# Performance work log

Measured on AMD Instinct MI355X. Metric: run time of the kernel, lower is better.

The kernel has to match this reference:

```python
import jax, jax.numpy as jnp
from jax import lax
import numpy as np

K = 5  # length_inter_tile
EPS = 0.01


def _conv(x, w, b):
    y = lax.conv_general_dilated(x, w, (1, 1), ((1, 1), (1, 1)),
                                 dimension_numbers=('NCHW', 'OIHW', 'NCHW'))
    return y + b[None, :, None, None]


def _leaky(x):
    return jnp.where(x >= 0, x, 0.01 * x)


def _unfold(x, k=K):
    # torch F.unfold(x, k, padding=k//2): (b,c,h,w) -> (b, c*k*k, h*w), channel-major ordering
    b, c, h, w = x.shape
    p = k // 2
    xp = jnp.pad(x, ((0, 0), (0, 0), (p, p), (p, p)))
    pat = jnp.stack([xp[:, :, i:i + h, j:j + w] for i in range(k) for j in range(k)], axis=2)
    return pat.reshape(b, c * k * k, h * w)


def _fold(x, c, h, w, k=K):
    # torch F.fold: (b, c*k*k, h*w) -> (b, c, h, w) with overlap-add, padding=k//2
    b = x.shape[0]
    p = k // 2
    xr = x.reshape(b, c, k, k, h, w)
    out = jnp.zeros((b, c, h + 2 * p, w + 2 * p), x.dtype)
    for i in range(k):
        for j in range(k):
            out = out.at[:, :, i:i + h, j:j + w].add(xr[:, :, i, j])
    return out[:, :, p:p + h, p:p + w]


def _mmn(x, axes):
    mn = jnp.min(x, axis=axes, keepdims=True)
    mx = jnp.max(x, axis=axes, keepdims=True)
    return (x - mn) / (mx - mn + 0.001)


def setup_inputs() -> dict:
    key = jax.random.key(0)
    ks = jax.random.split(key, 8)
    b, t, ch_in, h, w = 1, 16, 10, 24, 24
    t_de, ch_de = 16, 12
    sc = 0.02
    return {
        'x': jax.random.normal(ks[0], (b, t, ch_in, h, w), jnp.float32),
        'design': jax.random.uniform(ks[1], (b, t_de, ch_de, h, w), jnp.float32),
        'gt': jax.random.uniform(ks[2], (b, t_de, 3, h, w), jnp.float32),
        'w1': jax.random.normal(ks[3], (1024, 160, 3, 3), jnp.float32) * sc,
        'b1': jnp.zeros((1024,), jnp.float32),
        'w2': jax.random.normal(ks[4], (1024, 1024, 3, 3), jnp.float32) * sc,
        'b2': jnp.zeros((1024,), jnp.float32),
        'w3': jax.random.normal(ks[5], (1024, 1024, 3, 3), jnp.float32) * sc,
        'b3': jnp.zeros((1024,), jnp.float32),
        'wf': jax.random.normal(ks[6], (6400, 1024, 3, 3), jnp.float32) * sc,
        'bf': jnp.zeros((6400,), jnp.float32),
    }


def _forward(x, design, gt, w1, b1, w2, b2, w3, b3, wf, bf):
    b, t, ch_in, h, w = x.shape
    t_de, ch_de = design.shape[1], design.shape[2]
    hw = h * w
    N = K * K  # num_inter

    # unfold design: (b, t_de*ch_de*N, hw) -> (b*hw, N, t_de, ch_de)
    d = _unfold(design.reshape(b, t_de * ch_de, h, w))
    d = d.transpose(0, 2, 1).reshape(b * hw, t_de * ch_de, N)
    d = d.transpose(0, 2, 1).reshape(b * hw, N, t_de, ch_de)

    # norm in each prediction window (per channel-group, per sample)
    d = jnp.concatenate([
        d[..., 0:1],
        _mmn(d[..., 1:4], (1, 2, 3)),
        _mmn(d[..., 4:5], (1, 2)),
        _mmn(d[..., 5:8], (1, 2, 3)),
        _mmn(d[..., 8:], (1, 2)),  # each grid channel independently
    ], axis=-1)

    M = b * hw * N
    domain = d.reshape(M, t_de, ch_de)
    X = d[:, :, :t, :].reshape(M, t, ch_de)

    # feature network (n_layers=4 -> 3 leaky convs) + weight head
    f = _leaky(_conv(x.reshape(b, t * ch_in, h, w), w1, b1))
    f = _leaky(_conv(f, w2, b2))
    f = _leaky(_conv(f, w3, b3))
    Wt = jnp.tanh(_conv(f, wf, bf))  # (b, N*t*t, h, w)
    Wm = Wt.reshape(b, N, t, t, h, w).transpose(0, 4, 5, 1, 2, 3).reshape(M, t, t)
    Wm = jnp.einsum('nij,nkj->nik', Wm, Wm) + jnp.eye(t, dtype=Wm.dtype)

    XTW = jnp.einsum('ntc,ntu->ncu', X, Wm)          # (M, ch_de, t)
    XTWX = jnp.einsum('nct,ntd->ncd', XTW, X)        # (M, ch_de, ch_de)
    A = XTWX.reshape(b * hw, N, ch_de, ch_de).sum(1) + EPS * jnp.eye(ch_de, dtype=XTWX.dtype)

    # reference for loss (unfolded)
    ref = _unfold(gt.reshape(b, t_de * 3, h, w))
    ref = ref.transpose(0, 2, 1).reshape(b * hw, t_de * 3, N)
    ref = ref.transpose(0, 2, 1).reshape(M, t_de, 3)

    outs, folded = [], []
    for ch in range(3):
        Y = _unfold(x[:, :, ch])                      # (b, t*N, hw)
        Y = Y.transpose(0, 2, 1).reshape(b * hw, t, N)
        Y = Y.transpose(0, 2, 1).reshape(M, t, 1)
        XTWY = jnp.einsum('nct,nto->nco', XTW, Y)
        Bv = XTWY.reshape(b * hw, N, ch_de, 1).sum(1)
        para = jnp.linalg.solve(A, Bv)                # (b*hw, ch_de, 1)
        para_r = jnp.broadcast_to(para[:, None], (b * hw, N, ch_de, 1)).reshape(M, ch_de, 1)
        o = jnp.einsum('ntc,nco->nto', domain, para_r)  # (M, t_de, 1)
        outs.append(o[..., 0])
        # overlap-add fold of per-window predictions
        oc = o.reshape(b, hw, N, t_de).transpose(0, 3, 2, 1).reshape(b, t_de * N, hw)
        num = _fold(oc, t_de, h, w)
        den = _fold(jnp.ones_like(oc), t_de, h, w)
        folded.append(num / den)

    out_for_loss = jnp.stack(outs, axis=-1)           # (M, t_de, 3)
    out = jnp.stack(folded, axis=2)                   # (b, t_de, 3, h, w)
    loss = jnp.mean(jnp.abs(out_for_loss - ref))      # L1 stand-in for loss_for_stit_v1
    return out, loss


def reference(x, design, gt, w1, b1, w2, b2, w3, b3, wf, bf):
    return _forward(x, design, gt, w1, b1, w2, b2, w3, b3, wf, bf)
```

## Files before the change

### kernel.cpp

```cpp
#include <hip/hip_runtime.h>
#include <math.h>


typedef __attribute__((ext_vector_type(8))) short sh8;
typedef __attribute__((ext_vector_type(4))) float f32x4;

#define OFF_PART 0UL
#define OFF_X2T  58982400UL
#define OFF_WTT  58982400UL
#define OFF_ACT  85524480UL
#define OFF_DN   87883776UL
#define OFF_OB   98942976UL
#define OFF_MN   101707776UL
#define OFF_MX   101723904UL
#define OFF_LP   101740032UL


__device__ inline void glds16(const void* gsrc, void* ldst) {
    __builtin_amdgcn_global_load_lds((const __attribute__((address_space(1))) void*)gsrc,
                                     (__attribute__((address_space(3))) void*)ldst, 16, 0, 0);
}

__global__ __launch_bounds__(64) void minmax_kernel(const float* __restrict__ design,
                                                    float* __restrict__ mn_o,
                                                    float* __restrict__ mx_o) {
    int p = blockIdx.x;
    int py = p / 24, px = p % 24;
    int lane = threadIdx.x;
    float mn[7], mx[7];
#pragma unroll
    for (int g = 0; g < 7; g++) { mn[g] = 1e30f; mx[g] = -1e30f; }
    for (int e = lane; e < 400; e += 64) {
        int n = e / 16, td = e % 16;
        int yy = py + n / 5 - 2, xx = px + n % 5 - 2;
        bool ok = (yy >= 0 && yy < 24 && xx >= 0 && xx < 24);
#pragma unroll
        for (int cd = 1; cd < 12; cd++) {
            float v = ok ? design[(td * 12 + cd) * 576 + yy * 24 + xx] : 0.0f;
            int g = (cd <= 3) ? 0 : (cd == 4) ? 1 : (cd <= 7) ? 2 : 3 + (cd - 8);
            mn[g] = fminf(mn[g], v);
            mx[g] = fmaxf(mx[g], v);
        }
    }
#pragma unroll
    for (int s = 32; s >= 1; s >>= 1) {
#pragma unroll
        for (int g = 0; g < 7; g++) {
            mn[g] = fminf(mn[g], __shfl_xor(mn[g], s));
            mx[g] = fmaxf(mx[g], __shfl_xor(mx[g], s));
        }
    }
    if (lane == 0) {
#pragma unroll
        for (int g = 0; g < 7; g++) {
            mn_o[p * 7 + g] = mn[g];
            mx_o[p * 7 + g] = mx[g];
        }
    }
}

__global__ void dnorm_kernel(const float* __restrict__ design,
                             const float* __restrict__ mn,
                             const float* __restrict__ mx,
                             float* __restrict__ dn) {
    int idx = blockIdx.x * 256 + threadIdx.x;
    if (idx >= 14400 * 192) return;
    int cd = idx % 12;
    int td = (idx / 12) % 16;
    int n  = (idx / 192) % 25;
    int p  = idx / 4800;
    int py = p / 24, px = p % 24;
    int yy = py + n / 5 - 2, xx = px + n % 5 - 2;
    float v = (yy >= 0 && yy < 24 && xx >= 0 && xx < 24)
                  ? design[(td * 12 + cd) * 576 + yy * 24 + xx] : 0.0f;
    if (cd >= 1) {
        int g = (cd <= 3) ? 0 : (cd == 4) ? 1 : (cd <= 7) ? 2 : 3 + (cd - 8);
        float a = mn[p * 7 + g], b = mx[p * 7 + g];
        v = (v - a) / (b - a + 0.001f);
    }
    dn[idx] = v;
}

__global__ __launch_bounds__(256) void im2col_kernel(const float* __restrict__ act,
                                                     char* __restrict__ x2t, int nrows) {
    int row = blockIdx.x * 256 + threadIdx.x;
    if (row >= nrows) return;
    int kc = row / 576, px = row % 576;
    int y = px / 24, x = px % 24;
    int k0 = kc * 32;
    int ic = k0 / 9;
    int tap = k0 - ic * 9;
    sh8 hv[4], lv[4];
#pragma unroll
    for (int e = 0; e < 32; ++e) {
        int dy = tap / 3, dx = tap - dy * 3;
        int yy = y + dy - 1, xx = x + dx - 1;
        float v = (yy >= 0 && yy < 24 && xx >= 0 && xx < 24)
                      ? act[ic * 576 + yy * 24 + xx] : 0.0f;
        unsigned u = __builtin_bit_cast(unsigned, v);
        hv[e / 8][e % 8] = (short)(u >> 16);
        float fh = __builtin_bit_cast(float, u & 0xFFFF0000u);
        lv[e / 8][e % 8] = (short)(__builtin_bit_cast(unsigned, v - fh) >> 16);
        if (++tap == 9) { tap = 0; ++ic; }
    }
    char* dst = x2t + (long)kc * 92160 + (long)px * 80;
#pragma unroll
    for (int s4 = 0; s4 < 4; ++s4) {
        *(sh8*)(dst + s4 * 16) = hv[s4];
        *(sh8*)(dst + 46080 + s4 * 16) = lv[s4];
    }
}

__global__ void finalize_kernel(const float* __restrict__ part,
                                const float* __restrict__ bias,
                                float* __restrict__ act, int total, int nsplit) {
    int idx = blockIdx.x * 256 + threadIdx.x;
    if (idx >= total) return;
    float s = 0.0f;
    for (int k = 0; k < nsplit; k++) s += part[(long)k * total + idx];
    s += bias[idx / 576];
    act[idx] = s >= 0.0f ? s : 0.01f * s;
}

__global__ __launch_bounds__(256, 2)
void conv_mfma3_kernel(const char* __restrict__ x2t,
                       const float* __restrict__ wgt,
                       float* __restrict__ part,
                       int K, int cps, int cout) {
    __shared__ __align__(1024) char sA[16384];
    __shared__ __align__(1024) char sB[46080];

    const int tid = threadIdx.x;
    const int lane = tid & 63;
    const int w = tid >> 6;
    const int wo = w >> 1, wp = w & 1;
    const int q = lane >> 4, ln15 = lane & 15;
    const int ocb = blockIdx.x, pxh = blockIdx.y, s = blockIdx.z;
    const long K4 = (long)K * 4;
    const int c0 = s * cps;

    const int arow = lane >> 3;
    const int acol = (lane & 7) * 16;
    const int sw = (ln15 & 7) << 4;
    const int bbase = (wp * 144 + ln15) * 80 + q * 16;

    f32x4 acc[4][9];
#pragma unroll
    for (int a = 0; a < 4; ++a)
#pragma unroll
        for (int j = 0; j < 9; ++j) acc[a][j] = f32x4{0.f, 0.f, 0.f, 0.f};

#pragma unroll 1
    for (int cc = c0; cc < c0 + cps; ++cc) {
        __syncthreads();
        {
            const char* wsrc = (const char*)wgt + (long)(ocb * 128) * K4 + (long)cc * 128;
            for (int it = w; it < 16; it += 4) {
                int r = it * 8 + arow;
                glds16(wsrc + (long)r * K4 + (acol ^ ((r & 7) << 4)), sA + it * 1024);
            }
            const char* bsrc = x2t + (long)cc * 92160 + pxh * 23040;
            for (int it = w; it < 45; it += 4) {
                int boff = it * 1024 + lane * 16;
                const char* src = (boff < 23040) ? bsrc + boff
                                                 : bsrc + 46080 + (boff - 23040);
                glds16(src, sB + it * 1024);
            }
        }
        asm volatile("s_waitcnt vmcnt(0)" ::: "memory");
        __syncthreads();

        sh8 ah[4], al[4];
#pragma unroll
        for (int ot = 0; ot < 4; ++ot) {
            const char* ap = sA + (wo * 64 + ot * 16 + ln15) * 128;
            float4 a0 = *(const float4*)(ap + ((q * 32) ^ sw));
            float4 a1 = *(const float4*)(ap + ((q * 32 + 16) ^ sw));
            float av[8] = {a0.x, a0.y, a0.z, a0.w, a1.x, a1.y, a1.z, a1.w};
#pragma unroll
            for (int e = 0; e < 8; ++e) {
                unsigned u = __builtin_bit_cast(unsigned, av[e]);
                ah[ot][e] = (short)(u >> 16);
                float fh = __builtin_bit_cast(float, u & 0xFFFF0000u);
                al[ot][e] = (short)(__builtin_bit_cast(unsigned, av[e] - fh) >> 16);
            }
        }
#pragma unroll
        for (int j = 0; j < 9; ++j) {
            int ba = bbase + j * (16 * 80);
            sh8 bh = *(const sh8*)(sB + ba);
            sh8 bl = *(const sh8*)(sB + 23040 + ba);
#pragma unroll
            for (int ot = 0; ot < 4; ++ot) {
                acc[ot][j] = __builtin_amdgcn_mfma_f32_16x16x32_bf16(ah[ot], bh, acc[ot][j], 0, 0, 0);
                acc[ot][j] = __builtin_amdgcn_mfma_f32_16x16x32_bf16(al[ot], bh, acc[ot][j], 0, 0, 0);
                acc[ot][j] = __builtin_amdgcn_mfma_f32_16x16x32_bf16(ah[ot], bl, acc[ot][j], 0, 0, 0);
            }
        }
    }
#pragma unroll
    for (int ot = 0; ot < 4; ++ot) {
        int oc0 = ocb * 128 + wo * 64 + ot * 16 + q * 4;
#pragma unroll
        for (int j = 0; j < 9; ++j) {
            int px = pxh * 288 + wp * 144 + j * 16 + ln15;
#pragma unroll
            for (int vr = 0; vr < 4; ++vr)
                part[((long)s * cout + oc0 + vr) * 576 + px] = acc[ot][j][vr];
        }
    }
}

__global__ __launch_bounds__(256) void tanh_tr_kernel(const float* __restrict__ part,
                                                      const float* __restrict__ bias,
                                                      float* __restrict__ wtT) {
    __shared__ float tile[64][65];
    int oc0 = blockIdx.x * 64, p0 = blockIdx.y * 64;
    int tx = threadIdx.x, ty = threadIdx.y;
#pragma unroll
    for (int k = 0; k < 16; k++) {
        int row = ty + k * 4;
        float s = 0.f;
#pragma unroll
        for (int sp = 0; sp < 4; ++sp)
            s += part[((long)sp * 6400 + oc0 + row) * 576 + p0 + tx];
        tile[row][tx] = tanhf(s + bias[oc0 + row]);
    }
    __syncthreads();
#pragma unroll
    for (int k = 0; k < 16; k++) {
        int rr = ty + k * 4;
        wtT[(long)(p0 + rr) * 6400 + oc0 + tx] = tile[tx][rr];
    }
}

__global__ __launch_bounds__(256) void stagec_kernel(const float* __restrict__ dn,
                                                     const float* __restrict__ wtT,
                                                     const float* __restrict__ xin,
                                                     const float* __restrict__ gt,
                                                     float* __restrict__ ob,
                                                     float* __restrict__ lp) {
    int p = blockIdx.x;
    int py = p / 24, px = p % 24;
    int tid = threadIdx.x;
    __shared__ float sX[4800];
    __shared__ float sW[6400];
    __shared__ float sY[1200];
    __shared__ float sP[192];
    __shared__ float sXTW[192];
    __shared__ float sA[144];
    __shared__ float sB[36];
    __shared__ double dA[144];
    __shared__ double db[36];
    __shared__ float spara[36];
    __shared__ float sred[256];

    for (int e = tid; e < 4800; e += 256) sX[e] = dn[(long)p * 4800 + e];
    for (int e = tid; e < 6400; e += 256) sW[e] = wtT[(long)p * 6400 + e];
    for (int e = tid; e < 1200; e += 256) {
        int n = e / 48, t = (e % 48) / 3, ch = e % 3;
        int yy = py + n / 5 - 2, xx = px + n % 5 - 2;
        sY[e] = (yy >= 0 && yy < 24 && xx >= 0 && xx < 24)
                    ? xin[(t * 10 + ch) * 576 + yy * 24 + xx] : 0.0f;
    }
    if (tid < 144) sA[tid] = 0.0f;
    if (tid < 36) sB[tid] = 0.0f;
    __syncthreads();

    for (int n = 0; n < 25; n++) {
        const float* X = sX + n * 192;
        const float* W = sW + n * 256;
        if (tid < 192) {
            int c = tid >> 4, j = tid & 15;
            float s = 0.0f;
#pragma unroll
            for (int t = 0; t < 16; t++) s = fmaf(X[t * 12 + c], W[t * 16 + j], s);
            sP[tid] = s;
        }
        __syncthreads();
        if (tid < 192) {
            int c = tid >> 4, u = tid & 15;
            float s = X[u * 12 + c];
#pragma unroll
            for (int j = 0; j < 16; j++) s = fmaf(sP[c * 16 + j], W[u * 16 + j], s);
            sXTW[tid] = s;
        }
        __syncthreads();
        if (tid < 144) {
            int c = tid / 12, d2 = tid % 12;
            float s = 0.0f;
#pragma unroll
            for (int t = 0; t < 16; t++) s = fmaf(sXTW[c * 16 + t], X[t * 12 + d2], s);
            sA[tid] += s;
        } else if (tid < 180) {
            int e = tid - 144;
            int c = e / 3, ch = e % 3;
            float s = 0.0f;
#pragma unroll
            for (int t = 0; t < 16; t++) s = fmaf(sXTW[c * 16 + t], sY[n * 48 + t * 3 + ch], s);
            sB[e] += s;
        }
        __syncthreads();
    }

    if (tid < 144) dA[tid] = (double)sA[tid] + ((tid % 13 == 0) ? 0.01 : 0.0);
    if (tid < 36) db[tid] = (double)sB[tid];
    __syncthreads();

    if (tid == 0) {
        for (int kk = 0; kk < 12; kk++) {
            double d = dA[kk * 12 + kk];
            for (int q2 = 0; q2 < kk; q2++) d -= dA[kk * 12 + q2] * dA[kk * 12 + q2];
            d = sqrt(d);
            dA[kk * 12 + kk] = d;
            double inv = 1.0 / d;
            for (int i = kk + 1; i < 12; i++) {
                double s = dA[i * 12 + kk];
                for (int q2 = 0; q2 < kk; q2++) s -= dA[i * 12 + q2] * dA[kk * 12 + q2];
                dA[i * 12 + kk] = s * inv;
            }
        }
        for (int ch = 0; ch < 3; ch++) {
            double t2[12];
            for (int i = 0; i < 12; i++) {
                double s = db[i * 3 + ch];
                for (int q2 = 0; q2 < i; q2++) s -= dA[i * 12 + q2] * t2[q2];
                t2[i] = s / dA[i * 12 + i];
            }
            for (int i = 11; i >= 0; i--) {
                double s = t2[i];
                for (int q2 = i + 1; q2 < 12; q2++) s -= dA[q2 * 12 + i] * t2[q2];
                t2[i] = s / dA[i * 12 + i];
            }
            for (int i = 0; i < 12; i++) spara[i * 3 + ch] = (float)t2[i];
        }
    }
    __syncthreads();

    float lsum = 0.0f;
    for (int e = tid; e < 1200; e += 256) {
        int n = e / 48, td = (e % 48) / 3, ch = e % 3;
        float s = 0.0f;
#pragma unroll
        for (int c = 0; c < 12; c++) s = fmaf(sX[n * 192 + td * 12 + c], spara[c * 3 + ch], s);
        ob[((long)(p * 25 + n)) * 48 + td * 3 + ch] = s;
        int yy = py + n / 5 - 2, xx = px + n % 5 - 2;
        float rv = (yy >= 0 && yy < 24 && xx >= 0 && xx < 24)
                       ? gt[(td * 3 + ch) * 576 + yy * 24 + xx] : 0.0f;
        lsum += fabsf(s - rv);
    }
    sred[tid] = lsum;
    __syncthreads();
    for (int s = 128; s >= 1; s >>= 1) {
        if (tid < s) sred[tid] += sred[tid + s];
        __syncthreads();
    }
    if (tid == 0) lp[p] = sred[0];
}

__global__ void fold_kernel(const float* __restrict__ ob, float* __restrict__ out) {
    int idx = blockIdx.x * 256 + threadIdx.x;
    if (idx >= 27648) return;
    int td = idx / 1728;
    int rem = idx % 1728;
    int ch = rem / 576;
    int p = rem % 576;
    int y = p / 24, x = p % 24;
    float num = 0.0f;
    int den = 0;
    for (int i = 0; i < 5; i++) {
        int yy = y + 2 - i;
        if (yy < 0 || yy >= 24) continue;
        for (int j = 0; j < 5; j++) {
            int xx = x + 2 - j;
            if (xx < 0 || xx >= 24) continue;
            num += ob[((long)((yy * 24 + xx) * 25 + i * 5 + j)) * 48 + td * 3 + ch];
            den++;
        }
    }
    out[idx] = num / (float)den;
}

__global__ __launch_bounds__(64) void loss_kernel(const float* __restrict__ lp,
                                                  float* __restrict__ out) {
    int t = threadIdx.x;
    float s = 0.0f;
    for (int e = t; e < 576; e += 64) s += lp[e];
#pragma unroll
    for (int d = 32; d >= 1; d >>= 1) s += __shfl_xor(s, d);
    if (t == 0) out[27648] = s / 691200.0f;
}

extern "C" void kernel_launch(void* const* d_in, const int* in_sizes, int n_in,
                              void* d_out, int out_size, void* d_ws, size_t ws_size,
                              hipStream_t stream) {
    const float* x      = (const float*)d_in[0];
    const float* design = (const float*)d_in[1];
    const float* gt     = (const float*)d_in[2];
    const float* w1     = (const float*)d_in[3];
    const float* b1     = (const float*)d_in[4];
    const float* w2     = (const float*)d_in[5];
    const float* b2     = (const float*)d_in[6];
    const float* w3     = (const float*)d_in[7];
    const float* b3     = (const float*)d_in[8];
    const float* wf     = (const float*)d_in[9];
    const float* bf     = (const float*)d_in[10];
    float* out = (float*)d_out;
    char* wsb  = (char*)d_ws;

    float* part = (float*)(wsb + OFF_PART);
    char*  x2t  = wsb + OFF_X2T;
    float* wtT  = (float*)(wsb + OFF_WTT);
    float* act  = (float*)(wsb + OFF_ACT);
    float* dn   = (float*)(wsb + OFF_DN);
    float* ob   = (float*)(wsb + OFF_OB);
    float* mn   = (float*)(wsb + OFF_MN);
    float* mx   = (float*)(wsb + OFF_MX);
    float* lp   = (float*)(wsb + OFF_LP);

    minmax_kernel<<<576, 64, 0, stream>>>(design, mn, mx);
    dnorm_kernel<<<10800, 256, 0, stream>>>(design, mn, mx, dn);

    im2col_kernel<<<102, 256, 0, stream>>>(x, x2t, 45 * 576);
    conv_mfma3_kernel<<<dim3(8, 2, 15), 256, 0, stream>>>(x2t, w1, part, 1440, 3, 1024);
    finalize_kernel<<<2304, 256, 0, stream>>>(part, b1, act, 589824, 15);
    im2col_kernel<<<648, 256, 0, stream>>>(act, x2t, 288 * 576);
    conv_mfma3_kernel<<<dim3(8, 2, 16), 256, 0, stream>>>(x2t, w2, part, 9216, 18, 1024);
    finalize_kernel<<<2304, 256, 0, stream>>>(part, b2, act, 589824, 16);
    im2col_kernel<<<648, 256, 0, stream>>>(act, x2t, 288 * 576);
    conv_mfma3_kernel<<<dim3(8, 2, 16), 256, 0, stream>>>(x2t, w3, part, 9216, 18, 1024);
    finalize_kernel<<<2304, 256, 0, stream>>>(part, b3, act, 589824, 16);
    im2col_kernel<<<648, 256, 0, stream>>>(act, x2t, 288 * 576);
    conv_mfma3_kernel<<<dim3(50, 2, 4), 256, 0, stream>>>(x2t, wf, part, 9216, 72, 6400);
    tanh_tr_kernel<<<dim3(100, 9), dim3(64, 4), 0, stream>>>(part, bf, wtT);

    stagec_kernel<<<576, 256, 0, stream>>>(dn, wtT, x, gt, ob, lp);
    fold_kernel<<<108, 256, 0, stream>>>(ob, out);
    loss_kernel<<<1, 64, 0, stream>>>(lp, out);
}
```

Baseline: 550.8 us.

## Double-buffer weight tiles in conv MFMA kernel and swizzle final conv blocks across XCDs

The conv kernel now double-buffers the A (weight) tile in LDS, prefetching the next channel's weights while waiting only on the current tile's loads. This partially hides global-load latency. The MFMA loop is wrapped in s_setprio to favour compute waves. For the large final conv the launch becomes 1D, with a block-index remap that places blocks sharing an input pixel half and neighbouring output blocks on XCDs for better L2 reuse. Extra LDS (32KB more) may reduce occupancy, and the vmcnt(4) wait count must match the per-wave load count.

```diff
diff --git a/kernel.cpp b/kernel.cpp
--- a/kernel.cpp
+++ b/kernel.cpp
@@ -122,12 +122,13 @@
     act[idx] = s >= 0.0f ? s : 0.01f * s;
 }
 
+template<int SWZ>
 __global__ __launch_bounds__(256, 2)
-void conv_mfma3_kernel(const char* __restrict__ x2t,
+void conv_mfma4_kernel(const char* __restrict__ x2t,
                        const float* __restrict__ wgt,
                        float* __restrict__ part,
                        int K, int cps, int cout) {
-    __shared__ __align__(1024) char sA[16384];
+    __shared__ __align__(1024) char sA[2][16384];
     __shared__ __align__(1024) char sB[46080];
 
     const int tid = threadIdx.x;
@@ -135,7 +136,16 @@
     const int w = tid >> 6;
     const int wo = w >> 1, wp = w & 1;
     const int q = lane >> 4, ln15 = lane & 15;
-    const int ocb = blockIdx.x, pxh = blockIdx.y, s = blockIdx.z;
+
+    int ocb, pxh, s;
+    if (SWZ) {
+        int g = blockIdx.x;
+        int xcd = g & 7, slot = g >> 3;
+        int p = xcd + 8 * (slot >> 1);
+        ocb = p % 50; s = p / 50; pxh = slot & 1;
+    } else {
+        ocb = blockIdx.x; pxh = blockIdx.y; s = blockIdx.z;
+    }
     const long K4 = (long)K * 4;
     const int c0 = s * cps;
 
@@ -150,15 +160,21 @@
 #pragma unroll
         for (int j = 0; j < 9; ++j) acc[a][j] = f32x4{0.f, 0.f, 0.f, 0.f};
 
+    const char* wsrc0 = (const char*)wgt + (long)(ocb * 128) * K4;
+
+    {
+        const char* wsrc = wsrc0 + (long)c0 * 128;
+        for (int it = w; it < 16; it += 4) {
+            int r = it * 8 + arow;
+            glds16(wsrc + (long)r * K4 + (acol ^ ((r & 7) << 4)), sA[0] + it * 1024);
+        }
+    }
+
 #pragma unroll 1
-    for (int cc = c0; cc < c0 + cps; ++cc) {
+    for (int t = 0; t < cps; ++t) {
+        const int cc = c0 + t;
         __syncthreads();
         {
-            const char* wsrc = (const char*)wgt + (long)(ocb * 128) * K4 + (long)cc * 128;
-            for (int it = w; it < 16; it += 4) {
-                int r = it * 8 + arow;
-                glds16(wsrc + (long)r * K4 + (acol ^ ((r & 7) << 4)), sA + it * 1024);
-            }
             const char* bsrc = x2t + (long)cc * 92160 + pxh * 23040;
             for (int it = w; it < 45; it += 4) {
                 int boff = it * 1024 + lane * 16;
@@ -167,13 +183,24 @@
                 glds16(src, sB + it * 1024);
             }
         }
-        asm volatile("s_waitcnt vmcnt(0)" ::: "memory");
-        __syncthreads();
-
+        if (t + 1 < cps) {
+            const char* wsrc = wsrc0 + (long)(cc + 1) * 128;
+            char* dst = sA[(t + 1) & 1];
+            for (int it = w; it < 16; it += 4) {
+                int r = it * 8 + arow;
+                glds16(wsrc + (long)r * K4 + (acol ^ ((r & 7) << 4)), dst + it * 1024);
+            }
+            asm volatile("s_waitcnt vmcnt(4)" ::: "memory");
+        } else {
+            asm volatile("s_waitcnt vmcnt(0)" ::: "memory");
+        }
+        __syncthreads();
+
+        const char* sAc = sA[t & 1];
         sh8 ah[4], al[4];
 #pragma unroll
         for (int ot = 0; ot < 4; ++ot) {
-            const char* ap = sA + (wo * 64 + ot * 16 + ln15) * 128;
+            const char* ap = sAc + (wo * 64 + ot * 16 + ln15) * 128;
             float4 a0 = *(const float4*)(ap + ((q * 32) ^ sw));
             float4 a1 = *(const float4*)(ap + ((q * 32 + 16) ^ sw));
             float av[8] = {a0.x, a0.y, a0.z, a0.w, a1.x, a1.y, a1.z, a1.w};
@@ -185,6 +212,7 @@
                 al[ot][e] = (short)(__builtin_bit_cast(unsigned, av[e] - fh) >> 16);
             }
         }
+        __builtin_amdgcn_s_setprio(1);
 #pragma unroll
         for (int j = 0; j < 9; ++j) {
             int ba = bbase + j * (16 * 80);
@@ -197,6 +225,7 @@
                 acc[ot][j] = __builtin_amdgcn_mfma_f32_16x16x32_bf16(ah[ot], bl, acc[ot][j], 0, 0, 0);
             }
         }
+        __builtin_amdgcn_s_setprio(0);
     }
 #pragma unroll
     for (int ot = 0; ot < 4; ++ot) {
@@ -422,16 +451,16 @@
     dnorm_kernel<<<10800, 256, 0, stream>>>(design, mn, mx, dn);
 
     im2col_kernel<<<102, 256, 0, stream>>>(x, x2t, 45 * 576);
-    conv_mfma3_kernel<<<dim3(8, 2, 15), 256, 0, stream>>>(x2t, w1, part, 1440, 3, 1024);
+    conv_mfma4_kernel<0><<<dim3(8, 2, 15), 256, 0, stream>>>(x2t, w1, part, 1440, 3, 1024);
     finalize_kernel<<<2304, 256, 0, stream>>>(part, b1, act, 589824, 15);
     im2col_kernel<<<648, 256, 0, stream>>>(act, x2t, 288 * 576);
-    conv_mfma3_kernel<<<dim3(8, 2, 16), 256, 0, stream>>>(x2t, w2, part, 9216, 18, 1024);
+    conv_mfma4_kernel<0><<<dim3(8, 2, 16), 256, 0, stream>>>(x2t, w2, part, 9216, 18, 1024);
     finalize_kernel<<<2304, 256, 0, stream>>>(part, b2, act, 589824, 16);
     im2col_kernel<<<648, 256, 0, stream>>>(act, x2t, 288 * 576);
-    conv_mfma3_kernel<<<dim3(8, 2, 16), 256, 0, stream>>>(x2t, w3, part, 9216, 18, 1024);
+    conv_mfma4_kernel<0><<<dim3(8, 2, 16), 256, 0, stream>>>(x2t, w3, part, 9216, 18, 1024);
     finalize_kernel<<<2304, 256, 0, stream>>>(part, b3, act, 589824, 16);
     im2col_kernel<<<648, 256, 0, stream>>>(act, x2t, 288 * 576);
-    conv_mfma3_kernel<<<dim3(50, 2, 4), 256, 0, stream>>>(x2t, wf, part, 9216, 72, 6400);
+    conv_mfma4_kernel<1><<<400, 256, 0, stream>>>(x2t, wf, part, 9216, 72, 6400);
     tanh_tr_kernel<<<dim3(100, 9), dim3(64, 4), 0, stream>>>(part, bf, wtT);
 
     stagec_kernel<<<576, 256, 0, stream>>>(dn, wtT, x, gt, ob, lp);
```

Result: slower. 570.5 us (+3.6%).

## Double-buffer conv MFMA kernel with 512 threads and pre-split bf16 weights in LDS

Applied to the files above, without the earlier changes.

The conv GEMM kernel moves from 256 to 512 threads per block, each wave computing half as many output-channel tiles. LDS buffers for the activation and weight tiles are doubled so the next channel chunk is prefetched while MFMAs run on the current one. Weights are now loaded into registers, split into hi/lo bf16 once by the staging thread, and stored pre-split in LDS, instead of every wave re-splitting fp32 values after reading them. The final conv uses fewer K-splits (2 instead of 4), which shrinks the partial-sum buffer and the reduction work in tanh_tr, at the cost of fewer blocks and one block per CU.

```diff
diff --git a/kernel.cpp b/kernel.cpp
--- a/kernel.cpp
+++ b/kernel.cpp
@@ -6,14 +6,14 @@
 typedef __attribute__((ext_vector_type(4))) float f32x4;
 
 #define OFF_PART 0UL
-#define OFF_X2T  58982400UL
-#define OFF_WTT  58982400UL
-#define OFF_ACT  85524480UL
-#define OFF_DN   87883776UL
-#define OFF_OB   98942976UL
-#define OFF_MN   101707776UL
-#define OFF_MX   101723904UL
-#define OFF_LP   101740032UL
+#define OFF_X2T  37748736UL
+#define OFF_WTT  37748736UL
+#define OFF_ACT  64290816UL
+#define OFF_DN   66650112UL
+#define OFF_OB   77709312UL
+#define OFF_MN   80474112UL
+#define OFF_MX   80490240UL
+#define OFF_LP   80506368UL
 
 
 __device__ inline void glds16(const void* gsrc, void* ldst) {
@@ -122,13 +122,13 @@
     act[idx] = s >= 0.0f ? s : 0.01f * s;
 }
 
-__global__ __launch_bounds__(256, 2)
-void conv_mfma3_kernel(const char* __restrict__ x2t,
+__global__ __launch_bounds__(512, 1)
+void conv_mfma6_kernel(const char* __restrict__ x2t,
                        const float* __restrict__ wgt,
                        float* __restrict__ part,
                        int K, int cps, int cout) {
-    __shared__ __align__(1024) char sA[16384];
-    __shared__ __align__(1024) char sB[46080];
+    __shared__ __align__(1024) char sB[2][46080];
+    __shared__ __align__(1024) char sA[2][16384];
 
     const int tid = threadIdx.x;
     const int lane = tid & 63;
@@ -136,71 +136,113 @@
     const int wo = w >> 1, wp = w & 1;
     const int q = lane >> 4, ln15 = lane & 15;
     const int ocb = blockIdx.x, pxh = blockIdx.y, s = blockIdx.z;
-    const long K4 = (long)K * 4;
     const int c0 = s * cps;
 
-    const int arow = lane >> 3;
-    const int acol = (lane & 7) * 16;
-    const int sw = (ln15 & 7) << 4;
+    const int st_oc = tid >> 2;
+    const int kq = tid & 3;
+    const float* wrow = wgt + (long)(ocb * 128 + st_oc) * K + kq * 8;
+    const int wslot = (((kq) + (st_oc >> 1)) & 3) << 4;
+    char* const awr_hi0 = sA[0] + st_oc * 64 + wslot;
+
+    int aoff[2];
+#pragma unroll
+    for (int ot = 0; ot < 2; ++ot) {
+        int oc = wo * 32 + ot * 16 + ln15;
+        aoff[ot] = oc * 64 + (((q + (oc >> 1)) & 3) << 4);
+    }
     const int bbase = (wp * 144 + ln15) * 80 + q * 16;
 
-    f32x4 acc[4][9];
-#pragma unroll
-    for (int a = 0; a < 4; ++a)
+    f32x4 acc[2][9];
+#pragma unroll
+    for (int a = 0; a < 2; ++a)
 #pragma unroll
         for (int j = 0; j < 9; ++j) acc[a][j] = f32x4{0.f, 0.f, 0.f, 0.f};
 
+    {
+        const char* bsrc = x2t + (long)c0 * 92160 + pxh * 23040;
+        for (int it = w; it < 45; it += 8) {
+            int boff = it * 1024 + lane * 16;
+            const char* src = (boff < 23040) ? bsrc + boff
+                                             : bsrc + 46080 + (boff - 23040);
+            glds16(src, sB[0] + it * 1024);
+        }
+        const float* p = wrow + (long)c0 * 32;
+        float4 a0 = *(const float4*)(p);
+        float4 a1 = *(const float4*)(p + 4);
+        float av[8] = {a0.x, a0.y, a0.z, a0.w, a1.x, a1.y, a1.z, a1.w};
+        sh8 h8, l8;
+#pragma unroll
+        for (int e = 0; e < 8; ++e) {
+            unsigned u = __builtin_bit_cast(unsigned, av[e]);
+            h8[e] = (short)(u >> 16);
+            float fh = __builtin_bit_cast(float, u & 0xFFFF0000u);
+            l8[e] = (short)(__builtin_bit_cast(unsigned, av[e] - fh) >> 16);
+        }
+        *(sh8*)(awr_hi0) = h8;
+        *(sh8*)(awr_hi0 + 8192) = l8;
+    }
+    asm volatile("s_waitcnt vmcnt(0)" ::: "memory");
+    __syncthreads();
+
 #pragma unroll 1
-    for (int cc = c0; cc < c0 + cps; ++cc) {
-        __syncthreads();
-        {
-            const char* wsrc = (const char*)wgt + (long)(ocb * 128) * K4 + (long)cc * 128;
-            for (int it = w; it < 16; it += 4) {
-                int r = it * 8 + arow;
-                glds16(wsrc + (long)r * K4 + (acol ^ ((r & 7) << 4)), sA + it * 1024);
-            }
-            const char* bsrc = x2t + (long)cc * 92160 + pxh * 23040;
-            for (int it = w; it < 45; it += 4) {
+    for (int t = 0; t < cps; ++t) {
+        const int cur = t & 1;
+        const bool pf = (t + 1 < cps);
+        float4 a0, a1;
+        if (pf) {
+            const long cc1 = (long)(c0 + t + 1);
+            const char* bsrc = x2t + cc1 * 92160 + pxh * 23040;
+            char* bdst = sB[cur ^ 1];
+            for (int it = w; it < 45; it += 8) {
                 int boff = it * 1024 + lane * 16;
                 const char* src = (boff < 23040) ? bsrc + boff
                                                  : bsrc + 46080 + (boff - 23040);
-                glds16(src, sB + it * 1024);
-            }
-        }
-        asm volatile("s_waitcnt vmcnt(0)" ::: "memory");
-        __syncthreads();
-
-        sh8 ah[4], al[4];
-#pragma unroll
-        for (int ot = 0; ot < 4; ++ot) {
-            const char* ap = sA + (wo * 64 + ot * 16 + ln15) * 128;
-            float4 a0 = *(const float4*)(ap + ((q * 32) ^ sw));
-            float4 a1 = *(const float4*)(ap + ((q * 32 + 16) ^ sw));
-            float av[8] = {a0.x, a0.y, a0.z, a0.w, a1.x, a1.y, a1.z, a1.w};
-#pragma unroll
-            for (int e = 0; e < 8; ++e) {
-                unsigned u = __builtin_bit_cast(unsigned, av[e]);
-                ah[ot][e] = (short)(u >> 16);
-                float fh = __builtin_bit_cast(float, u & 0xFFFF0000u);
-                al[ot][e] = (short)(__builtin_bit_cast(unsigned, av[e] - fh) >> 16);
-            }
+                glds16(src, bdst + it * 1024);
+            }
+            const float* p = wrow + cc1 * 32;
+            a0 = *(const float4*)(p);
+            a1 = *(const float4*)(p + 4);
+        }
+        const char* sAc = sA[cur];
+        const char* sBc = sB[cur];
+        sh8 ah[2], al[2];
+#pragma unroll
+        for (int ot = 0; ot < 2; ++ot) {
+            ah[ot] = *(const sh8*)(sAc + aoff[ot]);
+            al[ot] = *(const sh8*)(sAc + 8192 + aoff[ot]);
         }
 #pragma unroll
         for (int j = 0; j < 9; ++j) {
-            int ba = bbase + j * (16 * 80);
-            sh8 bh = *(const sh8*)(sB + ba);
-            sh8 bl = *(const sh8*)(sB + 23040 + ba);
-#pragma unroll
-            for (int ot = 0; ot < 4; ++ot) {
+            int ba = bbase + j * 1280;
+            sh8 bh = *(const sh8*)(sBc + ba);
+            sh8 bl = *(const sh8*)(sBc + 23040 + ba);
+#pragma unroll
+            for (int ot = 0; ot < 2; ++ot) {
                 acc[ot][j] = __builtin_amdgcn_mfma_f32_16x16x32_bf16(ah[ot], bh, acc[ot][j], 0, 0, 0);
                 acc[ot][j] = __builtin_amdgcn_mfma_f32_16x16x32_bf16(al[ot], bh, acc[ot][j], 0, 0, 0);
                 acc[ot][j] = __builtin_amdgcn_mfma_f32_16x16x32_bf16(ah[ot], bl, acc[ot][j], 0, 0, 0);
             }
         }
-    }
-#pragma unroll
-    for (int ot = 0; ot < 4; ++ot) {
-        int oc0 = ocb * 128 + wo * 64 + ot * 16 + q * 4;
+        if (pf) {
+            asm volatile("s_waitcnt vmcnt(0)" ::: "memory");
+            float av[8] = {a0.x, a0.y, a0.z, a0.w, a1.x, a1.y, a1.z, a1.w};
+            sh8 h8, l8;
+#pragma unroll
+            for (int e = 0; e < 8; ++e) {
+                unsigned u = __builtin_bit_cast(unsigned, av[e]);
+                h8[e] = (short)(u >> 16);
+                float fh = __builtin_bit_cast(float, u & 0xFFFF0000u);
+                l8[e] = (short)(__builtin_bit_cast(unsigned, av[e] - fh) >> 16);
+            }
+            char* hb = sA[cur ^ 1] + st_oc * 64 + wslot;
+            *(sh8*)(hb) = h8;
+            *(sh8*)(hb + 8192) = l8;
+            __syncthreads();
+        }
+    }
+#pragma unroll
+    for (int ot = 0; ot < 2; ++ot) {
+        int oc0 = ocb * 128 + wo * 32 + ot * 16 + q * 4;
 #pragma unroll
         for (int j = 0; j < 9; ++j) {
             int px = pxh * 288 + wp * 144 + j * 16 + ln15;
@@ -213,7 +255,7 @@
 
 __global__ __launch_bounds__(256) void tanh_tr_kernel(const float* __restrict__ part,
                                                       const float* __restrict__ bias,
-                                                      float* __restrict__ wtT) {
+                                                      float* __restrict__ wtT, int nsplit) {
     __shared__ float tile[64][65];
     int oc0 = blockIdx.x * 64, p0 = blockIdx.y * 64;
     int tx = threadIdx.x, ty = threadIdx.y;
@@ -221,8 +263,7 @@
     for (int k = 0; k < 16; k++) {
         int row = ty + k * 4;
         float s = 0.f;
-#pragma unroll
-        for (int sp = 0; sp < 4; ++sp)
+        for (int sp = 0; sp < nsplit; ++sp)
             s += part[((long)sp * 6400 + oc0 + row) * 576 + p0 + tx];
         tile[row][tx] = tanhf(s + bias[oc0 + row]);
     }
@@ -422,17 +463,17 @@
     dnorm_kernel<<<10800, 256, 0, stream>>>(design, mn, mx, dn);
 
     im2col_kernel<<<102, 256, 0, stream>>>(x, x2t, 45 * 576);
-    conv_mfma3_kernel<<<dim3(8, 2, 15), 256, 0, stream>>>(x2t, w1, part, 1440, 3, 1024);
+    conv_mfma6_kernel<<<dim3(8, 2, 15), 512, 0, stream>>>(x2t, w1, part, 1440, 3, 1024);
     finalize_kernel<<<2304, 256, 0, stream>>>(part, b1, act, 589824, 15);
     im2col_kernel<<<648, 256, 0, stream>>>(act, x2t, 288 * 576);
-    conv_mfma3_kernel<<<dim3(8, 2, 16), 256, 0, stream>>>(x2t, w2, part, 9216, 18, 1024);
+    conv_mfma6_kernel<<<dim3(8, 2, 16), 512, 0, stream>>>(x2t, w2, part, 9216, 18, 1024);
     finalize_kernel<<<2304, 256, 0, stream>>>(part, b2, act, 589824, 16);
     im2col_kernel<<<648, 256, 0, stream>>>(act, x2t, 288 * 576);
-    conv_mfma3_kernel<<<dim3(8, 2, 16), 256, 0, stream>>>(x2t, w3, part, 9216, 18, 1024);
+    conv_mfma6_kernel<<<dim3(8, 2, 16), 512, 0, stream>>>(x2t, w3, part, 9216, 18, 1024);
     finalize_kernel<<<2304, 256, 0, stream>>>(part, b3, act, 589824, 16);
     im2col_kernel<<<648, 256, 0, stream>>>(act, x2t, 288 * 576);
-    conv_mfma3_kernel<<<dim3(50, 2, 4), 256, 0, stream>>>(x2t, wf, part, 9216, 72, 6400);
-    tanh_tr_kernel<<<dim3(100, 9), dim3(64, 4), 0, stream>>>(part, bf, wtT);
+    conv_mfma6_kernel<<<dim3(50, 2, 2), 512, 0, stream>>>(x2t, wf, part, 9216, 144, 6400);
+    tanh_tr_kernel<<<dim3(100, 9), dim3(64, 4), 0, stream>>>(part, bf, wtT, 2);
 
     stagec_kernel<<<576, 256, 0, stream>>>(dn, wtT, x, gt, ob, lp);
     fold_kernel<<<108, 256, 0, stream>>>(ob, out);
```

After: 663.0 us. +20.4%, slower.
